# Kernel optimization log

Measured on AMD Instinct MI355X. Metric: run time of the kernel, lower is better.

The kernel has to match this reference:

```python
import jax, jax.numpy as jnp
import numpy as np

B, S, E = 2, 2048, 2048
H, HKV, D = 32, 8, 64  # n_heads, n_kv_heads, head_dim


def _rope(x, cos, sin):
    # x: [B,S,h,D]; cos/sin: [1,S,1,D//2]. Complex rotate on (even,odd) pairs.
    xp = x.reshape(*x.shape[:-1], D // 2, 2)
    x0, x1 = xp[..., 0], xp[..., 1]
    r0 = x0 * cos - x1 * sin
    r1 = x0 * sin + x1 * cos
    return jnp.stack([r0, r1], axis=-1).reshape(x.shape)


def setup_inputs() -> dict:
    key = jax.random.key(0)
    ks = jax.random.split(key, 8)
    sc = 0.02
    # real RoPE frequencies (theta=10000) for realism
    inv = 1.0 / (10000.0 ** (np.arange(0, D, 2, dtype=np.float32) / D))
    t = np.arange(S, dtype=np.float32)
    ang = np.outer(t, inv)  # [S, D/2]
    return {
        "x": jax.random.normal(ks[0], (B, S, E), jnp.float32),
        "start_pos": 0,
        "freqs_cos": jnp.asarray(np.cos(ang))[None, :, None, :],
        "freqs_sin": jnp.asarray(np.sin(ang))[None, :, None, :],
        "wq": jax.random.normal(ks[1], (E, H * D), jnp.float32) * sc,
        "wk": jax.random.normal(ks[2], (E, HKV * D), jnp.float32) * sc,
        "wv": jax.random.normal(ks[3], (E, HKV * D), jnp.float32) * sc,
        "out_w": jax.random.normal(ks[4], (H * D, E), jnp.float32) * sc,
        "out_b": jnp.zeros((E,), jnp.float32),
        "k_cache": jnp.zeros((B, S, HKV, D), jnp.float32),
        "v_cache": jnp.zeros((B, S, HKV, D), jnp.float32),
    }


def reference(x, start_pos, freqs_cos, freqs_sin, wq, wk, wv, out_w, out_b, k_cache, v_cache):
    b, s, _ = x.shape
    q = (x @ wq).reshape(b, s, H, D)
    k = (x @ wk).reshape(b, s, HKV, D)
    v = (x @ wv).reshape(b, s, HKV, D)
    q = _rope(q, freqs_cos[:, :s], freqs_sin[:, :s])
    k = _rope(k, freqs_cos[:, :s], freqs_sin[:, :s])
    # KV-cache append (torch code detaches before writing)
    k_cache = jax.lax.dynamic_update_slice(k_cache, jax.lax.stop_gradient(k), (0, start_pos, 0, 0))
    v_cache = jax.lax.dynamic_update_slice(v_cache, jax.lax.stop_gradient(v), (0, start_pos, 0, 0))
    keys = k_cache[:b, : start_pos + s]    # [b, T, HKV, D]
    values = v_cache[:b, : start_pos + s]
    g = H // HKV
    if g > 1:  # GQA head repeat
        keys = jnp.repeat(keys, g, axis=2)     # [b, T, H, D]
        values = jnp.repeat(values, g, axis=2)
    scores = jnp.einsum("bqhd,bkhd->bhqk", q, keys) / jnp.sqrt(jnp.float32(D))
    att = jax.nn.softmax(scores, axis=-1)  # NOTE: source applies no causal mask
    o = jnp.einsum("bhqk,bkhd->bqhd", att, values).reshape(b, s, H * D)
    return o @ out_w + out_b
```

## Files before the change

### kernel.cpp

```cpp
#include <hip/hip_runtime.h>
#include <math.h>

#define B_    2
#define S_    2048
#define E_    2048
#define H_    32
#define HKV_  8
#define D_    64

typedef __bf16 bf16x8 __attribute__((ext_vector_type(8)));
typedef __bf16 bf16x4 __attribute__((ext_vector_type(4)));
typedef float  f32x4  __attribute__((ext_vector_type(4)));
typedef float  f32x16 __attribute__((ext_vector_type(16)));
typedef unsigned int u32x2 __attribute__((ext_vector_type(2)));
typedef unsigned int u32x4 __attribute__((ext_vector_type(4)));

#define GPTR(x) ((const __attribute__((address_space(1))) void*)(x))
#define LPTR(x) ((__attribute__((address_space(3))) void*)(x))

#define QK_SCALE_LOG2E 0.18033688011112042f

__global__ __launch_bounds__(256) void convert_kernel(
    const float* __restrict__ in, __bf16* __restrict__ out, int n8)
{
    const int i = blockIdx.x * 256 + threadIdx.x;
    if (i >= n8) return;
    const float4 a = ((const float4*)in)[i * 2];
    const float4 b = ((const float4*)in)[i * 2 + 1];
    bf16x8 o;
    o[0] = (__bf16)a.x; o[1] = (__bf16)a.y; o[2] = (__bf16)a.z; o[3] = (__bf16)a.w;
    o[4] = (__bf16)b.x; o[5] = (__bf16)b.y; o[6] = (__bf16)b.z; o[7] = (__bf16)b.w;
    ((bf16x8*)out)[i] = o;
}

__global__ __launch_bounds__(256) void transpose_convert_kernel(
    const float* __restrict__ in, __bf16* __restrict__ out, int K, int N)
{
    __shared__ float tile[32][33];
    const int k0 = blockIdx.y * 32, n0 = blockIdx.x * 32;
    const int r  = threadIdx.x >> 3;
    const int c4 = (threadIdx.x & 7) * 4;
    const float4 v = *(const float4*)&in[(size_t)(k0 + r) * N + n0 + c4];
    tile[r][c4 + 0] = v.x; tile[r][c4 + 1] = v.y;
    tile[r][c4 + 2] = v.z; tile[r][c4 + 3] = v.w;
    __syncthreads();
    ushort4 o;
    __bf16 h0 = (__bf16)tile[c4 + 0][r]; o.x = __builtin_bit_cast(unsigned short, h0);
    __bf16 h1 = (__bf16)tile[c4 + 1][r]; o.y = __builtin_bit_cast(unsigned short, h1);
    __bf16 h2 = (__bf16)tile[c4 + 2][r]; o.z = __builtin_bit_cast(unsigned short, h2);
    __bf16 h3 = (__bf16)tile[c4 + 3][r]; o.w = __builtin_bit_cast(unsigned short, h3);
    *(ushort4*)&out[(size_t)(n0 + r) * K + k0 + c4] = o;
}

__device__ __forceinline__ void gemm_mfma_body(
    const __bf16* __restrict__ A, const __bf16* __restrict__ Bt,
    int m0, int n0, int K, __bf16* sA, __bf16* sB, f32x4 acc[4][4])
{
    const int t    = threadIdx.x;
    const int w    = t >> 6;
    const int lane = t & 63;
    const int col  = lane & 15;
    const int quad = lane >> 4;
    const int wrow = (w >> 1) * 64;
    const int wcol = (w & 1) * 64;

    const int row0 = t >> 3;
    const int c0   = t & 7;

    for (int k0 = 0; k0 < K; k0 += 64) {
#pragma unroll
        for (int it = 0; it < 4; ++it) {
            const int row  = it * 32 + row0;
            const int csrc = c0 ^ (row & 7);
            __builtin_amdgcn_global_load_lds(
                GPTR(A + (size_t)(m0 + row) * K + k0 + csrc * 8),
                LPTR(sA + (it * 256 + t) * 8), 16, 0, 0);
        }
#pragma unroll
        for (int it = 0; it < 4; ++it) {
            const int row  = it * 32 + row0;
            const int csrc = c0 ^ (row & 7);
            __builtin_amdgcn_global_load_lds(
                GPTR(Bt + (size_t)(n0 + row) * K + k0 + csrc * 8),
                LPTR(sB + (it * 256 + t) * 8), 16, 0, 0);
        }
        __syncthreads();

#pragma unroll
        for (int kk = 0; kk < 2; ++kk) {
            bf16x8 af[4], bfr[4];
#pragma unroll
            for (int i = 0; i < 4; ++i) {
                const int m = wrow + i * 16 + col;
                af[i] = *(const bf16x8*)&sA[m * 64 + (((kk * 4 + quad) ^ (m & 7)) * 8)];
            }
#pragma unroll
            for (int j = 0; j < 4; ++j) {
                const int n = wcol + j * 16 + col;
                bfr[j] = *(const bf16x8*)&sB[n * 64 + (((kk * 4 + quad) ^ (n & 7)) * 8)];
            }
#pragma unroll
            for (int i = 0; i < 4; ++i)
#pragma unroll
                for (int j = 0; j < 4; ++j)
                    acc[i][j] = __builtin_amdgcn_mfma_f32_16x16x32_bf16(
                        af[i], bfr[j], acc[i][j], 0, 0, 0);
        }
        __syncthreads();
    }
}

__global__ __launch_bounds__(256) void gemm_qkv_kernel(
    const __bf16* __restrict__ xb, const __bf16* __restrict__ wT,
    __bf16* __restrict__ qb, __bf16* __restrict__ kb, __bf16* __restrict__ vb)
{
    __shared__ __bf16 sA[128 * 64];
    __shared__ __bf16 sB[128 * 64];
    f32x4 acc[4][4];
#pragma unroll
    for (int i = 0; i < 4; ++i)
#pragma unroll
        for (int j = 0; j < 4; ++j) acc[i][j] = (f32x4){0.f, 0.f, 0.f, 0.f};

    const int bx = blockIdx.x;
    const int m0 = blockIdx.y * 128;
    gemm_mfma_body(xb, wT, m0, bx * 128, E_, sA, sB, acc);

    __bf16* Cp; int ldc, nb;
    if (bx < 16)      { Cp = qb; ldc = H_ * D_;   nb = bx * 128; }
    else if (bx < 20) { Cp = kb; ldc = HKV_ * D_; nb = (bx - 16) * 128; }
    else              { Cp = vb; ldc = HKV_ * D_; nb = (bx - 20) * 128; }

    const float qsc = (bx < 16) ? QK_SCALE_LOG2E : 1.0f;

    const int lane = threadIdx.x & 63;
    const int col  = lane & 15;
    const int quad = lane >> 4;
    const int wrow = ((threadIdx.x >> 6) >> 1) * 64;
    const int wcol = ((threadIdx.x >> 6) & 1) * 64;
#pragma unroll
    for (int i = 0; i < 4; ++i)
#pragma unroll
        for (int j = 0; j < 4; ++j)
#pragma unroll
            for (int r = 0; r < 4; ++r) {
                const int m = m0 + wrow + i * 16 + quad * 4 + r;
                const int n = nb + wcol + j * 16 + col;
                Cp[(size_t)m * ldc + n] = (__bf16)(acc[i][j][r] * qsc);
            }
}

__global__ __launch_bounds__(256) void gemm_out_kernel(
    const __bf16* __restrict__ ob, const __bf16* __restrict__ woT,
    const float* __restrict__ bias, float* __restrict__ out)
{
    __shared__ __bf16 sA[128 * 64];
    __shared__ __bf16 sB[128 * 64];
    f32x4 acc[4][4];
#pragma unroll
    for (int i = 0; i < 4; ++i)
#pragma unroll
        for (int j = 0; j < 4; ++j) acc[i][j] = (f32x4){0.f, 0.f, 0.f, 0.f};

    const int m0 = blockIdx.y * 128;
    const int n0 = blockIdx.x * 128;
    gemm_mfma_body(ob, woT, m0, n0, H_ * D_, sA, sB, acc);

    const int lane = threadIdx.x & 63;
    const int col  = lane & 15;
    const int quad = lane >> 4;
    const int wrow = ((threadIdx.x >> 6) >> 1) * 64;
    const int wcol = ((threadIdx.x >> 6) & 1) * 64;
#pragma unroll
    for (int i = 0; i < 4; ++i)
#pragma unroll
        for (int j = 0; j < 4; ++j)
#pragma unroll
            for (int r = 0; r < 4; ++r) {
                const int m = m0 + wrow + i * 16 + quad * 4 + r;
                const int n = n0 + wcol + j * 16 + col;
                out[(size_t)m * E_ + n] = acc[i][j][r] + bias[n];
            }
}

__global__ __launch_bounds__(256) void rope_kernel(
    __bf16* __restrict__ p, const float* __restrict__ fc,
    const float* __restrict__ fs, int nh, int npairs)
{
    const int i = blockIdx.x * 256 + threadIdx.x;
    if (i >= npairs) return;
    const int pair = i & 31;
    const int row  = i >> 5;
    const int s    = (row / nh) % S_;
    const unsigned int v = ((const unsigned int*)p)[i];
    const float x0 = (float)__builtin_bit_cast(__bf16, (unsigned short)(v & 0xffff));
    const float x1 = (float)__builtin_bit_cast(__bf16, (unsigned short)(v >> 16));
    const float c  = fc[s * 32 + pair];
    const float sn = fs[s * 32 + pair];
    const __bf16 r0 = (__bf16)(x0 * c - x1 * sn);
    const __bf16 r1 = (__bf16)(x0 * sn + x1 * c);
    ((unsigned int*)p)[i] =
        ((unsigned int)__builtin_bit_cast(unsigned short, r1) << 16) |
        (unsigned int)__builtin_bit_cast(unsigned short, r0);
}

struct StageRegs {
    bf16x8  k0, k1;
    ushort4 va0, vc0, va1, vc1;
};

__device__ __forceinline__ void stage_load(
    StageRegs& r, const __bf16* kbase, const __bf16* vbase, int j0,
    int kkey, int kd, int vkp, int vdg)
{
    const int KSTR = HKV_ * D_;
    const __bf16* kr = kbase + (size_t)(j0 + kkey) * KSTR + kd;
    r.k0 = ((const bf16x8*)kr)[0];
    r.k1 = ((const bf16x8*)kr)[1];
    const __bf16* v0 = vbase + (size_t)(j0 + vkp) * KSTR + vdg;
    r.va0 = *(const ushort4*)(v0);
    r.vc0 = *(const ushort4*)(v0 + KSTR);
    r.va1 = *(const ushort4*)(v0 + 32);
    r.vc1 = *(const ushort4*)(v0 + KSTR + 32);
}

__device__ __forceinline__ void stage_write(
    const StageRegs& r, __bf16 (*sK)[72], __bf16 (*sVT)[72],
    int kkey, int kd, int vkp, int vdg)
{
    *(bf16x8*)&sK[kkey][kd]     = r.k0;
    *(bf16x8*)&sK[kkey][kd + 8] = r.k1;
    *(unsigned int*)&sVT[vdg + 0][vkp]      = ((unsigned)r.vc0.x << 16) | r.va0.x;
    *(unsigned int*)&sVT[vdg + 1][vkp]      = ((unsigned)r.vc0.y << 16) | r.va0.y;
    *(unsigned int*)&sVT[vdg + 2][vkp]      = ((unsigned)r.vc0.z << 16) | r.va0.z;
    *(unsigned int*)&sVT[vdg + 3][vkp]      = ((unsigned)r.vc0.w << 16) | r.va0.w;
    *(unsigned int*)&sVT[vdg + 32 + 0][vkp] = ((unsigned)r.vc1.x << 16) | r.va1.x;
    *(unsigned int*)&sVT[vdg + 32 + 1][vkp] = ((unsigned)r.vc1.y << 16) | r.va1.y;
    *(unsigned int*)&sVT[vdg + 32 + 2][vkp] = ((unsigned)r.vc1.z << 16) | r.va1.z;
    *(unsigned int*)&sVT[vdg + 32 + 3][vkp] = ((unsigned)r.vc1.w << 16) | r.va1.w;
}

__device__ __forceinline__ bf16x8 pack_pa(const f32x16& p, int i0)
{
    unsigned a0, a1, a2, a3;
    asm("v_cvt_pk_bf16_f32 %0, %1, %2" : "=v"(a0) : "v"(p[i0 + 0]), "v"(p[i0 + 1]));
    asm("v_cvt_pk_bf16_f32 %0, %1, %2" : "=v"(a1) : "v"(p[i0 + 2]), "v"(p[i0 + 3]));
    asm("v_cvt_pk_bf16_f32 %0, %1, %2" : "=v"(a2) : "v"(p[i0 + 4]), "v"(p[i0 + 5]));
    asm("v_cvt_pk_bf16_f32 %0, %1, %2" : "=v"(a3) : "v"(p[i0 + 6]), "v"(p[i0 + 7]));
    const u32x2 s02 = __builtin_amdgcn_permlane32_swap(a0, a2, false, false);
    const u32x2 s13 = __builtin_amdgcn_permlane32_swap(a1, a3, false, false);
    return __builtin_bit_cast(bf16x8, (u32x4){s02[0], s13[0], s02[1], s13[1]});
}

__device__ __forceinline__ void attn_tile(
    const __bf16 (*sK)[72], const __bf16 (*sVT)[72],
    const bf16x8* bQ, int lq, int hi,
    f32x16& O0, f32x16& O1, float& lsum)
{
    bf16x8 pa[4];
#pragma unroll
    for (int kb = 0; kb < 2; ++kb) {
        f32x16 p;
#pragma unroll
        for (int i = 0; i < 16; ++i) p[i] = 0.f;
        __builtin_amdgcn_s_setprio(1);
#pragma unroll
        for (int ks = 0; ks < 4; ++ks) {
            const bf16x8 aK = *(const bf16x8*)&sK[kb * 32 + lq][ks * 16 + hi * 8];
            p = __builtin_amdgcn_mfma_f32_32x32x16_bf16(aK, bQ[ks], p, 0, 0, 0);
        }
        __builtin_amdgcn_s_setprio(0);
        float ps = 0.f;
#pragma unroll
        for (int i = 0; i < 16; ++i) {
            p[i] = __builtin_amdgcn_exp2f(p[i]);
            ps += p[i];
        }
        lsum += ps;
        pa[kb * 2]     = pack_pa(p, 0);
        pa[kb * 2 + 1] = pack_pa(p, 8);
    }
    __builtin_amdgcn_s_setprio(1);
#pragma unroll
    for (int ks = 0; ks < 4; ++ks) {
        const bf16x8 vb0 = *(const bf16x8*)&sVT[lq][ks * 16 + hi * 8];
        const bf16x8 vb1 = *(const bf16x8*)&sVT[32 + lq][ks * 16 + hi * 8];
        O0 = __builtin_amdgcn_mfma_f32_32x32x16_bf16(pa[ks], vb0, O0, 0, 0, 0);
        O1 = __builtin_amdgcn_mfma_f32_32x32x16_bf16(pa[ks], vb1, O1, 0, 0, 0);
    }
    __builtin_amdgcn_s_setprio(0);
}

__global__ __launch_bounds__(256, 3) void attn_kernel(
    const __bf16* __restrict__ qw, const __bf16* __restrict__ kw,
    const __bf16* __restrict__ vw, __bf16* __restrict__ ow)
{
    __shared__ __bf16 sK0[64][72], sVT0[64][72];
    __shared__ __bf16 sK1[64][72], sVT1[64][72];

    const int t    = threadIdx.x;
    const int lane = t & 63;
    const int w    = t >> 6;
    const int lq   = lane & 31;
    const int hi   = lane >> 5;

    const int bh  = blockIdx.y;
    const int b   = bh >> 5;
    const int h   = bh & 31;
    const int kvh = h >> 2;
    const int q0  = blockIdx.x * 128 + w * 32;

    bf16x8 bQ[4];
    {
        const __bf16* qrow = qw + (((size_t)b * S_ + q0 + lq) * H_ + h) * D_;
#pragma unroll
        for (int ks = 0; ks < 4; ++ks)
            bQ[ks] = *(const bf16x8*)(qrow + ks * 16 + hi * 8);
    }

    f32x16 O0, O1;
#pragma unroll
    for (int i = 0; i < 16; ++i) { O0[i] = 0.f; O1[i] = 0.f; }
    float lsum = 0.f;

    const __bf16* kbase = kw + ((size_t)b * S_ * HKV_ + kvh) * D_;
    const __bf16* vbase = vw + ((size_t)b * S_ * HKV_ + kvh) * D_;
    const int kkey = t >> 2,        kd  = (t & 3) * 16;
    const int vkp  = (t & 31) * 2,  vdg = (t >> 5) * 4;

    StageRegs sr;
    stage_load(sr, kbase, vbase, 0, kkey, kd, vkp, vdg);
    stage_write(sr, sK0, sVT0, kkey, kd, vkp, vdg);
    __syncthreads();

#pragma unroll 1
    for (int j0 = 0; j0 < S_; j0 += 128) {
        StageRegs nx;
        stage_load(nx, kbase, vbase, j0 + 64, kkey, kd, vkp, vdg);
        attn_tile(sK0, sVT0, bQ, lq, hi, O0, O1, lsum);
        stage_write(nx, sK1, sVT1, kkey, kd, vkp, vdg);
        __syncthreads();
        if (j0 + 128 < S_)
            stage_load(nx, kbase, vbase, j0 + 128, kkey, kd, vkp, vdg);
        attn_tile(sK1, sVT1, bQ, lq, hi, O0, O1, lsum);
        if (j0 + 128 < S_)
            stage_write(nx, sK0, sVT0, kkey, kd, vkp, vdg);
        __syncthreads();
    }

    lsum += __shfl_xor(lsum, 32);
    const float inv = 1.0f / lsum;

#pragma unroll
    for (int r = 0; r < 16; ++r) {
        const int   qr = (r & 3) + 8 * (r >> 2) + 4 * hi;
        const float li = __shfl(inv, qr);
        __bf16* orow = ow + (((size_t)b * S_ + q0 + qr) * H_ + h) * D_;
        orow[lq]      = (__bf16)(O0[r] * li);
        orow[32 + lq] = (__bf16)(O1[r] * li);
    }
}

extern "C" void kernel_launch(void* const* d_in, const int* in_sizes, int n_in,
                              void* d_out, int out_size, void* d_ws, size_t ws_size,
                              hipStream_t stream)
{
    const float* x  = (const float*)d_in[0];
    const float* fc = (const float*)d_in[2];
    const float* fs = (const float*)d_in[3];
    const float* wq = (const float*)d_in[4];
    const float* wk = (const float*)d_in[5];
    const float* wv = (const float*)d_in[6];
    const float* wo = (const float*)d_in[7];
    const float* obias = (const float*)d_in[8];
    float* out = (float*)d_out;

    __bf16* ws  = (__bf16*)d_ws;
    __bf16* xb  = ws;
    __bf16* wT  = xb  + (size_t)4096 * 2048;
    __bf16* woT = wT  + (size_t)3072 * 2048;
    __bf16* qb  = woT + (size_t)2048 * 2048;
    __bf16* kb  = qb  + (size_t)B_ * S_ * H_ * D_;
    __bf16* vb  = kb  + (size_t)B_ * S_ * HKV_ * D_;
    __bf16* obf = vb  + (size_t)B_ * S_ * HKV_ * D_;

    convert_kernel<<<4096, 256, 0, stream>>>(x, xb, 4096 * 2048 / 8);
    transpose_convert_kernel<<<dim3(64, 64), 256, 0, stream>>>(wq, wT, E_, 2048);
    transpose_convert_kernel<<<dim3(16, 64), 256, 0, stream>>>(wk, wT + (size_t)2048 * 2048, E_, 512);
    transpose_convert_kernel<<<dim3(16, 64), 256, 0, stream>>>(wv, wT + (size_t)2560 * 2048, E_, 512);
    transpose_convert_kernel<<<dim3(64, 64), 256, 0, stream>>>(wo, woT, H_ * D_, E_);

    gemm_qkv_kernel<<<dim3(24, 32), 256, 0, stream>>>(xb, wT, qb, kb, vb);

    rope_kernel<<<(B_ * S_ * H_ * 32 + 255) / 256, 256, 0, stream>>>(
        qb, fc, fs, H_, B_ * S_ * H_ * 32);
    rope_kernel<<<(B_ * S_ * HKV_ * 32 + 255) / 256, 256, 0, stream>>>(
        kb, fc, fs, HKV_, B_ * S_ * HKV_ * 32);

    attn_kernel<<<dim3(S_ / 128, B_ * H_), 256, 0, stream>>>(qb, kb, vb, obf);

    gemm_out_kernel<<<dim3(16, 32), 256, 0, stream>>>(obf, woT, obias, out);
}
```

Before: 375.8 us.

## Fuse RoPE into QKV GEMM epilogue and merge weight transpose launches

New measurement: 494.8 us. +31.7%, slower.

```diff
diff --git a/kernel.cpp b/kernel.cpp
--- a/kernel.cpp
+++ b/kernel.cpp
@@ -9,7 +9,6 @@
 #define D_    64
 
 typedef __bf16 bf16x8 __attribute__((ext_vector_type(8)));
-typedef __bf16 bf16x4 __attribute__((ext_vector_type(4)));
 typedef float  f32x4  __attribute__((ext_vector_type(4)));
 typedef float  f32x16 __attribute__((ext_vector_type(16)));
 typedef unsigned int u32x2 __attribute__((ext_vector_type(2)));
@@ -33,11 +32,21 @@
     ((bf16x8*)out)[i] = o;
 }
 
-__global__ __launch_bounds__(256) void transpose_convert_kernel(
-    const float* __restrict__ in, __bf16* __restrict__ out, int K, int N)
-{
+__global__ __launch_bounds__(256) void transpose_convert_all_kernel(
+    const float* __restrict__ wq, const float* __restrict__ wk,
+    const float* __restrict__ wv, const float* __restrict__ wo,
+    __bf16* __restrict__ wT, __bf16* __restrict__ woT)
+{
+    const float* in; __bf16* out; int N, xb;
+    const int x = blockIdx.x;
+    if (x < 64)      { in = wq; out = wT;                        N = 2048; xb = x; }
+    else if (x < 80) { in = wk; out = wT + (size_t)2048 * 2048;  N = 512;  xb = x - 64; }
+    else if (x < 96) { in = wv; out = wT + (size_t)2560 * 2048;  N = 512;  xb = x - 80; }
+    else             { in = wo; out = woT;                       N = 2048; xb = x - 96; }
+    const int K = 2048;
+
     __shared__ float tile[32][33];
-    const int k0 = blockIdx.y * 32, n0 = blockIdx.x * 32;
+    const int k0 = blockIdx.y * 32, n0 = xb * 32;
     const int r  = threadIdx.x >> 3;
     const int c4 = (threadIdx.x & 7) * 4;
     const float4 v = *(const float4*)&in[(size_t)(k0 + r) * N + n0 + c4];
@@ -112,6 +121,7 @@
 
 __global__ __launch_bounds__(256) void gemm_qkv_kernel(
     const __bf16* __restrict__ xb, const __bf16* __restrict__ wT,
+    const float* __restrict__ fc, const float* __restrict__ fs,
     __bf16* __restrict__ qb, __bf16* __restrict__ kb, __bf16* __restrict__ vb)
 {
     __shared__ __bf16 sA[128 * 64];
@@ -131,7 +141,8 @@
     else if (bx < 20) { Cp = kb; ldc = HKV_ * D_; nb = (bx - 16) * 128; }
     else              { Cp = vb; ldc = HKV_ * D_; nb = (bx - 20) * 128; }
 
-    const float qsc = (bx < 16) ? QK_SCALE_LOG2E : 1.0f;
+    const bool  doRope = (bx < 20);
+    const float qsc    = (bx < 16) ? QK_SCALE_LOG2E : 1.0f;
 
     const int lane = threadIdx.x & 63;
     const int col  = lane & 15;
@@ -146,7 +157,17 @@
             for (int r = 0; r < 4; ++r) {
                 const int m = m0 + wrow + i * 16 + quad * 4 + r;
                 const int n = nb + wcol + j * 16 + col;
-                Cp[(size_t)m * ldc + n] = (__bf16)(acc[i][j][r] * qsc);
+                float val = acc[i][j][r] * qsc;
+                if (doRope) {
+                    const int   s    = m & (S_ - 1);
+                    const int   pair = (n & 63) >> 1;
+                    const float c    = fc[s * 32 + pair];
+                    const float sn   = fs[s * 32 + pair];
+                    const float oth  = __shfl_xor(val, 1);
+                    val = (lane & 1) ? (oth * sn + val * c)
+                                     : (val * c - oth * sn);
+                }
+                Cp[(size_t)m * ldc + n] = (__bf16)val;
             }
 }
 
@@ -181,27 +202,6 @@
                 const int n = n0 + wcol + j * 16 + col;
                 out[(size_t)m * E_ + n] = acc[i][j][r] + bias[n];
             }
-}
-
-__global__ __launch_bounds__(256) void rope_kernel(
-    __bf16* __restrict__ p, const float* __restrict__ fc,
-    const float* __restrict__ fs, int nh, int npairs)
-{
-    const int i = blockIdx.x * 256 + threadIdx.x;
-    if (i >= npairs) return;
-    const int pair = i & 31;
-    const int row  = i >> 5;
-    const int s    = (row / nh) % S_;
-    const unsigned int v = ((const unsigned int*)p)[i];
-    const float x0 = (float)__builtin_bit_cast(__bf16, (unsigned short)(v & 0xffff));
-    const float x1 = (float)__builtin_bit_cast(__bf16, (unsigned short)(v >> 16));
-    const float c  = fc[s * 32 + pair];
-    const float sn = fs[s * 32 + pair];
-    const __bf16 r0 = (__bf16)(x0 * c - x1 * sn);
-    const __bf16 r1 = (__bf16)(x0 * sn + x1 * c);
-    ((unsigned int*)p)[i] =
-        ((unsigned int)__builtin_bit_cast(unsigned short, r1) << 16) |
-        (unsigned int)__builtin_bit_cast(unsigned short, r0);
 }
 
 struct StageRegs {
@@ -291,7 +291,7 @@
     __builtin_amdgcn_s_setprio(0);
 }
 
-__global__ __launch_bounds__(256, 3) void attn_kernel(
+__global__ __launch_bounds__(256, 4) void attn_kernel(
     const __bf16* __restrict__ qw, const __bf16* __restrict__ kw,
     const __bf16* __restrict__ vw, __bf16* __restrict__ ow)
 {
@@ -385,17 +385,10 @@
     __bf16* obf = vb  + (size_t)B_ * S_ * HKV_ * D_;
 
     convert_kernel<<<4096, 256, 0, stream>>>(x, xb, 4096 * 2048 / 8);
-    transpose_convert_kernel<<<dim3(64, 64), 256, 0, stream>>>(wq, wT, E_, 2048);
-    transpose_convert_kernel<<<dim3(16, 64), 256, 0, stream>>>(wk, wT + (size_t)2048 * 2048, E_, 512);
-    transpose_convert_kernel<<<dim3(16, 64), 256, 0, stream>>>(wv, wT + (size_t)2560 * 2048, E_, 512);
-    transpose_convert_kernel<<<dim3(64, 64), 256, 0, stream>>>(wo, woT, H_ * D_, E_);
-
-    gemm_qkv_kernel<<<dim3(24, 32), 256, 0, stream>>>(xb, wT, qb, kb, vb);
-
-    rope_kernel<<<(B_ * S_ * H_ * 32 + 255) / 256, 256, 0, stream>>>(
-        qb, fc, fs, H_, B_ * S_ * H_ * 32);
-    rope_kernel<<<(B_ * S_ * HKV_ * 32 + 255) / 256, 256, 0, stream>>>(
-        kb, fc, fs, HKV_, B_ * S_ * HKV_ * 32);
+    transpose_convert_all_kernel<<<dim3(160, 64), 256, 0, stream>>>(
+        wq, wk, wv, wo, wT, woT);
+
+    gemm_qkv_kernel<<<dim3(24, 32), 256, 0, stream>>>(xb, wT, fc, fs, qb, kb, vb);
 
     attn_kernel<<<dim3(S_ / 128, B_ * H_), 256, 0, stream>>>(qb, kb, vb, obf);
 
```
